# Kernel optimization log

Measured on AMD Instinct MI355X. Metric: run time of the kernel, lower is better.

Reference implementation:

```python
import jax, jax.numpy as jnp
import numpy as np

B, S, H, D_LLM = 16, 4096, 1024, 4096
MEM_EVERY = 64
M = S // MEM_EVERY  # 64 mem tokens per row -> static max_mem_tokens
MEM_ID = 50279
VOCAB = 50280
LN_EPS = 1e-5


def setup_inputs() -> dict:
    key = jax.random.key(0)
    k1, k2, k3 = jax.random.split(key, 3)
    hidden = jax.random.normal(k1, (B, S, H), dtype=jnp.float32)
    gamma = jnp.ones((H,), jnp.float32)
    beta = jnp.zeros((H,), jnp.float32)
    # xavier-uniform-ish projection weight
    limit = float(np.sqrt(6.0 / (H + D_LLM)))
    W = jax.random.uniform(k2, (D_LLM, H), jnp.float32, -limit, limit)
    b = jnp.zeros((D_LLM,), jnp.float32)
    ids = jax.random.randint(k3, (B, S), 0, MEM_ID, dtype=jnp.int64)
    # place a mem token every MEM_EVERY positions (M per row)
    ids = ids.at[:, MEM_EVERY - 1::MEM_EVERY].set(MEM_ID)
    return {"hidden": hidden, "gamma": gamma, "beta": beta, "W": W, "b": b,
            "input_ids": ids, "mem_token_id": MEM_ID}


def reference(hidden, gamma, beta, W, b, input_ids, mem_token_id):
    # hidden: [B,S,H] last_hidden_state from the (external) Mamba backbone
    mask = input_ids == mem_token_id                      # [B,S]
    # LayerNorm per token (identical math to LN on gathered tokens only)
    mu = jnp.mean(hidden, axis=-1, keepdims=True)
    var = jnp.mean(jnp.square(hidden - mu), axis=-1, keepdims=True)
    normed = (hidden - mu) * jax.lax.rsqrt(var + LN_EPS) * gamma + beta  # [B,S,H]
    # scatter mem tokens into zero-padded buffer, preserving per-row order
    pos_in_row = jnp.cumsum(mask, axis=1) - 1             # [B,S] 0..M-1 at mem slots
    idx = jnp.where(mask, pos_in_row, M)                  # non-mem -> trash slot M
    b_idx = jnp.arange(hidden.shape[0])[:, None]
    buf = jnp.zeros((hidden.shape[0], M + 1, hidden.shape[-1]), hidden.dtype)
    buf = buf.at[b_idx, idx].set(normed)                  # [B,M+1,H]
    memory_features = buf[:, :M]                          # [B,M,H] zero-padded
    # linear projection to LLM input size
    return jnp.einsum('bmh,dh->bmd', memory_features, W) + b  # [B,M,D_LLM]
```

## Files before the change

### kernel.cpp

```cpp
#include <hip/hip_runtime.h>
#include <hip/hip_bf16.h>

#define Bn 16
#define Sn 4096
#define Hn 1024
#define Dn 4096
#define Mn 64
#define LN_EPS 1e-5f

typedef float f32x4 __attribute__((ext_vector_type(4)));
typedef short bf16x8 __attribute__((ext_vector_type(8)));

__device__ __forceinline__ unsigned short f2bf(float f) {
    union { float f; unsigned u; } in; in.f = f;
    unsigned u = in.u;
    return (unsigned short)((u + 0x7fffu + ((u >> 16) & 1u)) >> 16);
}

__global__ void scan_pos(const int* __restrict__ ids,
                         const int* __restrict__ memid_p,
                         int* __restrict__ pos) {
    const int b = blockIdx.x;
    const int t = threadIdx.x;
    const int memid = *memid_p;
    __shared__ int counts[256];
    __shared__ int offs[256];

    for (int m = t; m < Mn; m += 256) pos[b * Mn + m] = -1;

    const int CH = Sn / 256;
    const int* row = ids + (size_t)b * Sn;
    int local[CH];
    int cnt = 0;
    #pragma unroll
    for (int i = 0; i < CH; ++i) {
        int s = t * CH + i;
        if (row[s] == memid) local[cnt++] = s;
    }
    counts[t] = cnt;
    __syncthreads();
    if (t == 0) {
        int acc = 0;
        for (int i = 0; i < 256; ++i) { offs[i] = acc; acc += counts[i]; }
    }
    __syncthreads();
    int base = offs[t];
    for (int i = 0; i < cnt; ++i) {
        int m = base + i;
        if (m < Mn) pos[b * Mn + m] = local[i];
    }
}

__global__ void ln_gather(const float* __restrict__ hidden,
                          const float* __restrict__ gamma,
                          const float* __restrict__ beta,
                          const int* __restrict__ pos,
                          unsigned short* __restrict__ A) {
    const int r = blockIdx.x;
    const int b = r / Mn;
    const int t = threadIdx.x;
    unsigned short* arow = A + (size_t)r * Hn;
    const int s = pos[r];
    if (s < 0) {
        ushort4 z = make_ushort4(0, 0, 0, 0);
        ((ushort4*)arow)[t] = z;
        return;
    }
    const float* x = hidden + ((size_t)b * Sn + s) * Hn;
    float4 v = ((const float4*)x)[t];
    float sum = v.x + v.y + v.z + v.w;
    float sq  = v.x * v.x + v.y * v.y + v.z * v.z + v.w * v.w;
    #pragma unroll
    for (int o = 32; o >= 1; o >>= 1) {
        sum += __shfl_down(sum, o, 64);
        sq  += __shfl_down(sq,  o, 64);
    }
    __shared__ float s_sum[4], s_sq[4];
    int wave = t >> 6, lane = t & 63;
    if (lane == 0) { s_sum[wave] = sum; s_sq[wave] = sq; }
    __syncthreads();
    float tot   = s_sum[0] + s_sum[1] + s_sum[2] + s_sum[3];
    float totsq = s_sq[0]  + s_sq[1]  + s_sq[2]  + s_sq[3];
    float mu   = tot * (1.0f / Hn);
    float var  = totsq * (1.0f / Hn) - mu * mu;
    float rstd = rsqrtf(var + LN_EPS);
    float4 g  = ((const float4*)gamma)[t];
    float4 be = ((const float4*)beta)[t];
    ushort4 o16;
    o16.x = f2bf((v.x - mu) * rstd * g.x + be.x);
    o16.y = f2bf((v.y - mu) * rstd * g.y + be.y);
    o16.z = f2bf((v.z - mu) * rstd * g.z + be.z);
    o16.w = f2bf((v.w - mu) * rstd * g.w + be.w);
    ((ushort4*)arow)[t] = o16;
}

__global__ void cast_w(const float* __restrict__ W, unsigned short* __restrict__ Wb) {
    size_t i = (size_t)blockIdx.x * blockDim.x + threadIdx.x;
    float4 v = ((const float4*)W)[i];
    ushort4 o;
    o.x = f2bf(v.x); o.y = f2bf(v.y); o.z = f2bf(v.z); o.w = f2bf(v.w);
    ((ushort4*)Wb)[i] = o;
}

__global__ __launch_bounds__(256) void gemm_bt(
        const unsigned short* __restrict__ A,
        const unsigned short* __restrict__ Wb,
        const float* __restrict__ bias,
        float* __restrict__ C) {
    __shared__ unsigned short As[64 * 32];
    __shared__ unsigned short Bs[128 * 32];
    const int K = Hn;
    const int tid  = threadIdx.x;
    const int wave = tid >> 6;
    const int lane = tid & 63;
    const int mtile = blockIdx.y;
    const int ntile = blockIdx.x;
    const unsigned short* Abase = A  + (size_t)mtile * 64 * K;
    const unsigned short* Bbase = Wb + (size_t)ntile * 128 * K;

    const int rsub = lane >> 2;
    const int kb   = (lane & 3) * 8;
    const int quad = lane >> 4, l15 = lane & 15;

    f32x4 acc[4][2] = {};

    for (int k0 = 0; k0 < K; k0 += 32) {
        __syncthreads();
        {
            int row = wave * 16 + rsub;
            const unsigned short* ga = Abase + (size_t)row * K + k0 + kb;
            __builtin_amdgcn_global_load_lds(
                (const __attribute__((address_space(1))) void*)ga,
                (__attribute__((address_space(3))) void*)(As + wave * 512), 16, 0, 0);
        }
        #pragma unroll
        for (int c = 0; c < 2; ++c) {
            int chunk = wave * 2 + c;
            int row = chunk * 16 + rsub;
            const unsigned short* gb = Bbase + (size_t)row * K + k0 + kb;
            __builtin_amdgcn_global_load_lds(
                (const __attribute__((address_space(1))) void*)gb,
                (__attribute__((address_space(3))) void*)(Bs + chunk * 512), 16, 0, 0);
        }
        __syncthreads();

        bf16x8 af[4], bfr[2];
        #pragma unroll
        for (int i = 0; i < 4; ++i)
            af[i] = *(const bf16x8*)(As + (16 * i + l15) * 32 + quad * 8);
        #pragma unroll
        for (int j = 0; j < 2; ++j)
            bfr[j] = *(const bf16x8*)(Bs + (wave * 32 + 16 * j + l15) * 32 + quad * 8);
        #pragma unroll
        for (int i = 0; i < 4; ++i)
            #pragma unroll
            for (int j = 0; j < 2; ++j)
                acc[i][j] = __builtin_amdgcn_mfma_f32_16x16x32_bf16(
                                af[i], bfr[j], acc[i][j], 0, 0, 0);
    }

    const int crow = mtile * 64;
    const int ccol = ntile * 128 + wave * 32;
    #pragma unroll
    for (int j = 0; j < 2; ++j) {
        int col = ccol + 16 * j + l15;
        float bv = bias[col];
        #pragma unroll
        for (int i = 0; i < 4; ++i) {
            int r0 = crow + 16 * i + quad * 4;
            float* cp = C + (size_t)r0 * Dn + col;
            #pragma unroll
            for (int rg = 0; rg < 4; ++rg)
                cp[(size_t)rg * Dn] = acc[i][j][rg] + bv;
        }
    }
}

extern "C" void kernel_launch(void* const* d_in, const int* in_sizes, int n_in,
                              void* d_out, int out_size, void* d_ws, size_t ws_size,
                              hipStream_t stream) {
    const float* hidden = (const float*)d_in[0];
    const float* gamma  = (const float*)d_in[1];
    const float* beta   = (const float*)d_in[2];
    const float* W      = (const float*)d_in[3];
    const float* bias   = (const float*)d_in[4];
    const int*   ids    = (const int*)d_in[5];
    const int*   memid  = (const int*)d_in[6];
    float* out = (float*)d_out;

    char* ws = (char*)d_ws;
    int* pos = (int*)ws;
    unsigned short* Abf = (unsigned short*)(ws + 4096);
    unsigned short* Wbf = (unsigned short*)(ws + 4096 + (size_t)Bn * Mn * Hn * 2);

    scan_pos <<<Bn, 256, 0, stream>>>(ids, memid, pos);
    ln_gather<<<Bn * Mn, 256, 0, stream>>>(hidden, gamma, beta, pos, Abf);
    cast_w   <<<(Dn * Hn / 4) / 256, 256, 0, stream>>>(W, Wbf);
    gemm_bt  <<<dim3(Dn / 128, (Bn * Mn) / 64), 256, 0, stream>>>(Abf, Wbf, bias, out);
}
```

Before: 342.4 us.

## Fuse scan, LayerNorm gather and weight cast into one prep kernel

Merges the position scan, LayerNorm gather and W bf16 cast into a single launch. Each LN block recomputes the memory-token scan for its row and picks its own position through shared memory, which removes the pos workspace buffer. Extra blocks in the same grid handle the weight cast, so it can overlap with the gather. This cuts two kernel launches and inter-kernel dependencies, at the cost of redundant per-block scans of the id row.

```diff
diff --git a/kernel.cpp b/kernel.cpp
--- a/kernel.cpp
+++ b/kernel.cpp
@@ -17,16 +17,34 @@
     return (unsigned short)((u + 0x7fffu + ((u >> 16) & 1u)) >> 16);
 }
 
-__global__ void scan_pos(const int* __restrict__ ids,
-                         const int* __restrict__ memid_p,
-                         int* __restrict__ pos) {
-    const int b = blockIdx.x;
+__global__ __launch_bounds__(256) void prep(
+        const float* __restrict__ hidden,
+        const float* __restrict__ gamma,
+        const float* __restrict__ beta,
+        const float* __restrict__ W,
+        const int* __restrict__ ids,
+        const int* __restrict__ memid_p,
+        unsigned short* __restrict__ A,
+        unsigned short* __restrict__ Wb) {
     const int t = threadIdx.x;
+
+    if (blockIdx.x >= (unsigned)(Bn * Mn)) {
+        size_t i = (size_t)(blockIdx.x - Bn * Mn) * 256 + t;
+        float4 v = ((const float4*)W)[i];
+        ushort4 o;
+        o.x = f2bf(v.x); o.y = f2bf(v.y); o.z = f2bf(v.z); o.w = f2bf(v.w);
+        ((ushort4*)Wb)[i] = o;
+        return;
+    }
+
+    const int r = blockIdx.x;
+    const int b = r >> 6;
+    const int m = r & 63;
     const int memid = *memid_p;
+
     __shared__ int counts[256];
     __shared__ int offs[256];
-
-    for (int m = t; m < Mn; m += 256) pos[b * Mn + m] = -1;
+    __shared__ int s_pos;
 
     const int CH = Sn / 256;
     const int* row = ids + (size_t)b * Sn;
@@ -38,6 +56,7 @@
         if (row[s] == memid) local[cnt++] = s;
     }
     counts[t] = cnt;
+    if (t == 0) s_pos = -1;
     __syncthreads();
     if (t == 0) {
         int acc = 0;
@@ -45,22 +64,11 @@
     }
     __syncthreads();
     int base = offs[t];
-    for (int i = 0; i < cnt; ++i) {
-        int m = base + i;
-        if (m < Mn) pos[b * Mn + m] = local[i];
-    }
-}
+    if (base <= m && m < base + cnt) s_pos = local[m - base];
+    __syncthreads();
+    const int s = s_pos;
 
-__global__ void ln_gather(const float* __restrict__ hidden,
-                          const float* __restrict__ gamma,
-                          const float* __restrict__ beta,
-                          const int* __restrict__ pos,
-                          unsigned short* __restrict__ A) {
-    const int r = blockIdx.x;
-    const int b = r / Mn;
-    const int t = threadIdx.x;
     unsigned short* arow = A + (size_t)r * Hn;
-    const int s = pos[r];
     if (s < 0) {
         ushort4 z = make_ushort4(0, 0, 0, 0);
         ((ushort4*)arow)[t] = z;
@@ -92,14 +100,6 @@
     o16.z = f2bf((v.z - mu) * rstd * g.z + be.z);
     o16.w = f2bf((v.w - mu) * rstd * g.w + be.w);
     ((ushort4*)arow)[t] = o16;
-}
-
-__global__ void cast_w(const float* __restrict__ W, unsigned short* __restrict__ Wb) {
-    size_t i = (size_t)blockIdx.x * blockDim.x + threadIdx.x;
-    float4 v = ((const float4*)W)[i];
-    ushort4 o;
-    o.x = f2bf(v.x); o.y = f2bf(v.y); o.z = f2bf(v.z); o.w = f2bf(v.w);
-    ((ushort4*)Wb)[i] = o;
 }
 
 __global__ __launch_bounds__(256) void gemm_bt(
@@ -189,12 +189,10 @@
     float* out = (float*)d_out;
 
     char* ws = (char*)d_ws;
-    int* pos = (int*)ws;
-    unsigned short* Abf = (unsigned short*)(ws + 4096);
-    unsigned short* Wbf = (unsigned short*)(ws + 4096 + (size_t)Bn * Mn * Hn * 2);
+    unsigned short* Abf = (unsigned short*)ws;
+    unsigned short* Wbf = (unsigned short*)(ws + (size_t)Bn * Mn * Hn * 2);
 
-    scan_pos <<<Bn, 256, 0, stream>>>(ids, memid, pos);
-    ln_gather<<<Bn * Mn, 256, 0, stream>>>(hidden, gamma, beta, pos, Abf);
-    cast_w   <<<(Dn * Hn / 4) / 256, 256, 0, stream>>>(W, Wbf);
-    gemm_bt  <<<dim3(Dn / 128, (Bn * Mn) / 64), 256, 0, stream>>>(Abf, Wbf, bias, out);
+    prep   <<<Bn * Mn + Dn * Hn / 1024, 256, 0, stream>>>(hidden, gamma, beta, W,
+                                                          ids, memid, Abf, Wbf);
+    gemm_bt<<<dim3(Dn / 128, (Bn * Mn) / 64), 256, 0, stream>>>(Abf, Wbf, bias, out);
 }
```

After: 335.2 us. 1.02x faster.
